# Kernel tuning notes

Measured on AMD Instinct MI355X. Metric: run time of the kernel, lower is better.

The kernel has to match this reference:

```python
import jax, jax.numpy as jnp
import numpy as np

HEAD, STACK = 8, 2
EPS = 1e-5


def _ln2d(x):
    # F.layer_norm(x, x.size()[1:]): normalize over (seq, feature) jointly, no affine
    m = jnp.mean(x, axis=(1, 2), keepdims=True)
    v = jnp.var(x, axis=(1, 2), keepdims=True)
    return (x - m) / jnp.sqrt(v + EPS)


def setup_inputs() -> dict:
    key = jax.random.key(0)
    ks = jax.random.split(key, 8)
    B, S, V, E, D, C = 64, 1024, 8000, 200, 200, 31
    g = lambda k, shape, sc: (jax.random.normal(k, shape, jnp.float32) * sc)
    return dict(
        x=jax.random.randint(ks[0], (B, S), 0, V),
        embed=g(ks[1], (V, E), 0.02),
        pos=g(ks[2], (S, E), 0.02),
        Wp=g(ks[3], (E, D), 0.05), bp=jnp.zeros((D,), jnp.float32),
        Wm=g(ks[4], (D * HEAD, D), 0.05), bm=jnp.zeros((D,), jnp.float32),
        W1=g(ks[5], (D, D), 0.05), b1=jnp.zeros((D,), jnp.float32),
        W2=g(ks[6], (D, D), 0.05), b2=jnp.zeros((D,), jnp.float32),
        Wd=g(ks[7], (D, C), 0.05), bd=jnp.zeros((C,), jnp.float32),
    )


def reference(x, embed, pos, Wp, bp, Wm, bm, W1, b1, W2, b2, Wd, bd):
    h = embed[x] + pos                       # [B,S,200]
    scale = jnp.sqrt(jnp.asarray(Wp.shape[1], jnp.float32))
    for _ in range(STACK):                   # weights shared across stacks (aliased in torch)
        r = h
        p = h @ Wp + bp                      # q = k = v (same aliased Linear in torch)
        a = jax.nn.softmax(jnp.einsum('bsd,btd->bst', p, p) / scale, axis=-1)
        c = jnp.einsum('bst,btd->bsd', a, p)  # [B,S,200]
        cat = jnp.tile(c, (1, 1, HEAD))       # all heads identical -> concat = tile
        h = _ln2d(cat @ Wm + bm + r)
        r = h
        ff = jax.nn.relu(h @ W1 + b1) @ W2 + b2
        h = _ln2d(ff + r)
    return h[:, -1, :] @ Wd + bd             # [B, class_num]; dropout = identity (eval)
```

## Files before the change

kernel.cpp:

```cpp
#include <hip/hip_runtime.h>
#include <cstddef>
#include <cstdint>
#include <cmath>

#define BDIM  64
#define SDIM  1024
#define DDIM  200
#define DPAD  224
#define PSTRIDE 232
#define CDIM  31
#define NSTACK 2
#define EPS   1e-5f
#define LN_N  204800.0f

typedef __attribute__((ext_vector_type(8))) short short8;
typedef __attribute__((ext_vector_type(4))) short short4_t;
typedef __attribute__((ext_vector_type(4))) float f32x4;

__device__ __forceinline__ short f2bf(float f) {
    union { float f; unsigned u; } v; v.f = f;
    unsigned r = v.u + 0x7FFFu + ((v.u >> 16) & 1u);
    return (short)(r >> 16);
}
__device__ __forceinline__ float bf2f(short s) {
    union { unsigned u; float f; } v; v.u = ((unsigned)(unsigned short)s) << 16;
    return v.f;
}
__device__ __forceinline__ unsigned cvtpk_bf16(float a, float b) {
    unsigned r;
    asm volatile("v_cvt_pk_bf16_f32 %0, %1, %2" : "=v"(r) : "v"(a), "v"(b));
    return r;
}
__device__ __forceinline__ void gload_lds16(const short* g, short* l) {
    __builtin_amdgcn_global_load_lds(
        (const __attribute__((address_space(1))) void*)g,
        (__attribute__((address_space(3))) void*)l, 16, 0, 0);
}

__global__ void prep_kernel(const float* __restrict__ Wp, const float* __restrict__ bp,
                            const float* __restrict__ Wm, const float* __restrict__ bm,
                            const float* __restrict__ W1, const float* __restrict__ b1,
                            const float* __restrict__ W2, const float* __restrict__ b2,
                            short* __restrict__ WtP, short* __restrict__ WtM,
                            short* __restrict__ Wt1, short* __restrict__ Wt2,
                            float* __restrict__ bpP, float* __restrict__ bmP,
                            float* __restrict__ b1P, float* __restrict__ b2P,
                            float* __restrict__ csP, float* __restrict__ cs1)
{
    int idx = blockIdx.x * 256 + threadIdx.x;
    if (idx >= DPAD * DPAD) return;
    int n = idx / DPAD, k = idx - n * DPAD;
    bool valid = (n < DDIM) && (k < DDIM);
    WtP[idx] = valid ? f2bf(Wp[(size_t)k * DDIM + n]) : 0;
    Wt1[idx] = valid ? f2bf(W1[(size_t)k * DDIM + n]) : 0;
    Wt2[idx] = valid ? f2bf(W2[(size_t)k * DDIM + n]) : 0;
    float s = 0.f;
    if (valid) {
        #pragma unroll
        for (int blk = 0; blk < 8; ++blk)
            s += Wm[(size_t)(blk * DDIM + k) * DDIM + n];
    }
    WtM[idx] = valid ? f2bf(s) : 0;
    if (idx < DPAD) {
        bpP[idx] = idx < DDIM ? bp[idx] : 0.f;
        bmP[idx] = idx < DDIM ? bm[idx] : 0.f;
        b1P[idx] = idx < DDIM ? b1[idx] : 0.f;
        b2P[idx] = idx < DDIM ? b2[idx] : 0.f;
        float sp = 0.f, s1 = 0.f;
        if (idx < DDIM) {
            for (int kk = 0; kk < DDIM; ++kk) {
                sp += bf2f(f2bf(Wp[(size_t)kk * DDIM + idx]));
                s1 += bf2f(f2bf(W1[(size_t)kk * DDIM + idx]));
            }
        }
        csP[idx] = sp;
        cs1[idx] = s1;
    }
}

__global__ void embed_kernel(const int* __restrict__ x, const float* __restrict__ embed,
                             const float* __restrict__ pos, short* __restrict__ h)
{
    const int total = BDIM * SDIM * (DPAD / 4);
    for (int i = blockIdx.x * 256 + threadIdx.x; i < total; i += gridDim.x * 256) {
        const int row = i / (DPAD / 4);
        const int n0  = (i - row * (DPAD / 4)) * 4;
        short4_t o;
        if (n0 >= DDIM) {
            o[0] = o[1] = o[2] = o[3] = 0;
        } else {
            const int s = row & (SDIM - 1);
            const int tok = x[row];
            const float4 e  = *(const float4*)(embed + (size_t)tok * DDIM + n0);
            const float4 p4 = *(const float4*)(pos + (size_t)s * DDIM + n0);
            o[0] = f2bf(e.x + p4.x); o[1] = f2bf(e.y + p4.y);
            o[2] = f2bf(e.z + p4.z); o[3] = f2bf(e.w + p4.w);
        }
        *(short4_t*)(h + (size_t)row * DPAD + n0) = o;
    }
}

#define WSLICE 7168
__global__ __launch_bounds__(256, 3)
void gemm_bf(const short* __restrict__ act, const float* __restrict__ actParts,
             const short* __restrict__ Wt, const float* __restrict__ bias,
             const float* __restrict__ csW,
             const short* __restrict__ res, const float* __restrict__ resParts,
             short* __restrict__ out, float* __restrict__ parts,
             int doRelu, int outStride)
{
    __shared__ short WB[2][WSLICE];

    const int tid  = threadIdx.x;
    const int wave = tid >> 6, lane = tid & 63;
    const int lo   = lane & 15, hi = lane >> 4;
    const int mblk = blockIdx.x * 128;
    const int m0   = mblk + wave * 32;

    auto stage = [&](int ks, int buf) {
        for (int c = wave; c < 14; c += 4) {
            int row = c * 16 + (lane >> 2);
            int kc  = (lane & 3) ^ ((row >> 1) & 3);
            gload_lds16(Wt + (size_t)row * DPAD + ks * 32 + kc * 8,
                        &WB[buf][c * 512 + lane * 8]);
        }
    };

    f32x4 acc[2][14];
    #pragma unroll
    for (int mt = 0; mt < 2; ++mt)
        #pragma unroll
        for (int nt = 0; nt < 14; ++nt) acc[mt][nt] = (f32x4){0.f, 0.f, 0.f, 0.f};

    short8 af[2], afn[2];
    #pragma unroll
    for (int mt = 0; mt < 2; ++mt)
        af[mt] = *(const short8*)(act + (size_t)(m0 + mt * 16 + lo) * DPAD + hi * 8);
    stage(0, 0);
    __syncthreads();

    #pragma unroll
    for (int ks = 0; ks < 7; ++ks) {
        const int cur = ks & 1;
        if (ks < 6) {
            #pragma unroll
            for (int mt = 0; mt < 2; ++mt)
                afn[mt] = *(const short8*)(act + (size_t)(m0 + mt * 16 + lo) * DPAD
                                           + (ks + 1) * 32 + hi * 8);
            stage(ks + 1, cur ^ 1);
        }
        #pragma unroll
        for (int nt = 0; nt < 14; ++nt) {
            int brow = nt * 16 + lo;
            short8 bf_ = *(const short8*)&WB[cur][brow * 32
                                                  + ((hi * 8) ^ (((brow >> 1) & 3) << 3))];
            acc[0][nt] = __builtin_amdgcn_mfma_f32_16x16x32_bf16(af[0], bf_, acc[0][nt], 0, 0, 0);
            acc[1][nt] = __builtin_amdgcn_mfma_f32_16x16x32_bf16(af[1], bf_, acc[1][nt], 0, 0, 0);
        }
        __syncthreads();
        if (ks < 6) { af[0] = afn[0]; af[1] = afn[1]; }
    }

    const int bb = mblk >> 10;
    float inv_a = 1.f, corr = 0.f;
    if (actParts) {
        float mean = actParts[bb * 2] / LN_N;
        inv_a = rsqrtf(actParts[bb * 2 + 1] / LN_N - mean * mean + EPS);
        corr = mean * inv_a;
    }
    float mean_r = 0.f, inv_r = 1.f;
    if (resParts) {
        mean_r = resParts[bb * 2] / LN_N;
        inv_r = rsqrtf(resParts[bb * 2 + 1] / LN_N - mean_r * mean_r + EPS);
    }

    float s = 0.f, s2 = 0.f;
    #pragma unroll
    for (int mt = 0; mt < 2; ++mt) {
        #pragma unroll
        for (int nt = 0; nt < 14; ++nt) {
            const int n = nt * 16 + lo;
            const float bn = bias[n];
            const float cw = actParts ? csW[n] : 0.f;
            float v[4];
            #pragma unroll
            for (int r = 0; r < 4; ++r)
                v[r] = acc[mt][nt][r] * inv_a + bn - corr * cw;
            if (res) {
                #pragma unroll
                for (int r = 0; r < 4; ++r) {
                    int m = m0 + mt * 16 + hi * 4 + r;
                    v[r] += (bf2f(res[(size_t)m * DPAD + n]) - mean_r) * inv_r;
                }
            }
            if (doRelu)
                #pragma unroll
                for (int r = 0; r < 4; ++r) v[r] = fmaxf(v[r], 0.f);
            if (n >= DDIM)
                #pragma unroll
                for (int r = 0; r < 4; ++r) v[r] = 0.f;
            if (parts)
                #pragma unroll
                for (int r = 0; r < 4; ++r) { s += v[r]; s2 = fmaf(v[r], v[r], s2); }
            #pragma unroll
            for (int r = 0; r < 4; ++r) {
                int m = m0 + mt * 16 + hi * 4 + r;
                out[(size_t)m * outStride + n] = f2bf(v[r]);
            }
        }
    }

    if (parts) {
        __shared__ float rs[4], rq[4];
        #pragma unroll
        for (int off = 32; off; off >>= 1) {
            s  += __shfl_down(s, off);
            s2 += __shfl_down(s2, off);
        }
        if (lane == 0) { rs[wave] = s; rq[wave] = s2; }
        __syncthreads();
        if (tid == 0) {
            atomicAdd(&parts[bb * 2],     rs[0] + rs[1] + rs[2] + rs[3]);
            atomicAdd(&parts[bb * 2 + 1], rq[0] + rq[1] + rq[2] + rq[3]);
        }
    }
}

#define Y1S 232
__global__ __launch_bounds__(256, 2)
void ffn_bf(const short* __restrict__ act, const float* __restrict__ actParts,
            const float* __restrict__ csW1,
            const short* __restrict__ Wt1, const float* __restrict__ b1,
            const short* __restrict__ Wt2, const float* __restrict__ b2,
            short* __restrict__ out, float* __restrict__ parts)
{
    __shared__ short WB[2][WSLICE];
    __shared__ short Y1[64 * Y1S];

    const int tid  = threadIdx.x;
    const int wave = tid >> 6, lane = tid & 63;
    const int lo   = lane & 15, hi = lane >> 4;
    const int mblk = blockIdx.x * 64;
    const int m0   = mblk + wave * 16;
    const int bb   = mblk >> 10;

    auto stageW = [&](const short* W, int ks, int buf) {
        for (int c = wave; c < 14; c += 4) {
            int row = c * 16 + (lane >> 2);
            int kc  = (lane & 3) ^ ((row >> 1) & 3);
            gload_lds16(W + (size_t)row * DPAD + ks * 32 + kc * 8,
                        &WB[buf][c * 512 + lane * 8]);
        }
    };

    const float mean_a = actParts[bb * 2] / LN_N;
    const float inv_a  = rsqrtf(actParts[bb * 2 + 1] / LN_N - mean_a * mean_a + EPS);
    const float corr   = mean_a * inv_a;

    f32x4 acc[14];
    #pragma unroll
    for (int nt = 0; nt < 14; ++nt) acc[nt] = (f32x4){0.f, 0.f, 0.f, 0.f};

    short8 af = *(const short8*)(act + (size_t)(m0 + lo) * DPAD + hi * 8);
    short8 afn;
    stageW(Wt1, 0, 0);
    __syncthreads();

    #pragma unroll
    for (int ks = 0; ks < 7; ++ks) {
        const int cur = ks & 1;
        if (ks < 6) {
            afn = *(const short8*)(act + (size_t)(m0 + lo) * DPAD + (ks + 1) * 32 + hi * 8);
            stageW(Wt1, ks + 1, cur ^ 1);
        } else {
            stageW(Wt2, 0, cur ^ 1);
        }
        #pragma unroll
        for (int nt = 0; nt < 14; ++nt) {
            int brow = nt * 16 + lo;
            short8 bf_ = *(const short8*)&WB[cur][brow * 32
                                                  + ((hi * 8) ^ (((brow >> 1) & 3) << 3))];
            acc[nt] = __builtin_amdgcn_mfma_f32_16x16x32_bf16(af, bf_, acc[nt], 0, 0, 0);
        }
        __syncthreads();
        if (ks < 6) af = afn;
    }

    #pragma unroll
    for (int nt = 0; nt < 14; ++nt) {
        const int n = nt * 16 + lo;
        const float bn = b1[n];
        const float cw = csW1[n];
        #pragma unroll
        for (int r = 0; r < 4; ++r) {
            float v = fmaxf(acc[nt][r] * inv_a + bn - corr * cw, 0.f);
            Y1[(wave * 16 + hi * 4 + r) * Y1S + n] = f2bf(v);
        }
    }
    __syncthreads();

    #pragma unroll
    for (int nt = 0; nt < 14; ++nt) acc[nt] = (f32x4){0.f, 0.f, 0.f, 0.f};

    #pragma unroll
    for (int ks = 0; ks < 7; ++ks) {
        const int cur = (ks + 1) & 1;
        if (ks < 6) stageW(Wt2, ks + 1, cur ^ 1);
        short8 a2 = *(const short8*)&Y1[(wave * 16 + lo) * Y1S + ks * 32 + hi * 8];
        #pragma unroll
        for (int nt = 0; nt < 14; ++nt) {
            int brow = nt * 16 + lo;
            short8 bf_ = *(const short8*)&WB[cur][brow * 32
                                                  + ((hi * 8) ^ (((brow >> 1) & 3) << 3))];
            acc[nt] = __builtin_amdgcn_mfma_f32_16x16x32_bf16(a2, bf_, acc[nt], 0, 0, 0);
        }
        __syncthreads();
    }

    float s = 0.f, s2 = 0.f;
    #pragma unroll
    for (int nt = 0; nt < 14; ++nt) {
        const int n = nt * 16 + lo;
        const float bn = b2[n];
        float v[4];
        #pragma unroll
        for (int r = 0; r < 4; ++r) {
            int m = m0 + hi * 4 + r;
            v[r] = acc[nt][r] + bn + (bf2f(act[(size_t)m * DPAD + n]) - mean_a) * inv_a;
        }
        if (n >= DDIM)
            #pragma unroll
            for (int r = 0; r < 4; ++r) v[r] = 0.f;
        #pragma unroll
        for (int r = 0; r < 4; ++r) { s += v[r]; s2 = fmaf(v[r], v[r], s2); }
        #pragma unroll
        for (int r = 0; r < 4; ++r) {
            int m = m0 + hi * 4 + r;
            out[(size_t)m * DPAD + n] = f2bf(v[r]);
        }
    }

    {
        __shared__ float rs[4], rq[4];
        #pragma unroll
        for (int off = 32; off; off >>= 1) {
            s  += __shfl_down(s, off);
            s2 += __shfl_down(s2, off);
        }
        if (lane == 0) { rs[wave] = s; rq[wave] = s2; }
        __syncthreads();
        if (tid == 0) {
            atomicAdd(&parts[bb * 2],     rs[0] + rs[1] + rs[2] + rs[3]);
            atomicAdd(&parts[bb * 2 + 1], rq[0] + rq[1] + rq[2] + rq[3]);
        }
    }
}

__global__ void vt_kernel(const short* __restrict__ p, short* __restrict__ pt)
{
    __shared__ short T[32][33];
    const int b  = blockIdx.z;
    const int s0 = blockIdx.x * 32;
    const int d0 = blockIdx.y * 32;
    const int t  = threadIdx.x;
    const int row = t >> 3, c4 = (t & 7) * 4;
    short4_t v = *(const short4_t*)(p + ((size_t)b * SDIM + s0 + row) * PSTRIDE + d0 + c4);
    #pragma unroll
    for (int j = 0; j < 4; ++j) T[row][c4 + j] = v[j];
    __syncthreads();
    short4_t o;
    #pragma unroll
    for (int j = 0; j < 4; ++j) o[j] = T[c4 + j][row];
    *(short4_t*)(pt + ((size_t)b * DPAD + d0 + row) * SDIM + s0 + c4) = o;
}

__global__ __launch_bounds__(256, 2)
void attn_kernel(const short* __restrict__ pbf, const short* __restrict__ pt,
                 short* __restrict__ c, float qscale)
{
    __shared__ short Kbuf[2][7680];
    __shared__ short Vbuf[2][6656];

    const int bid = blockIdx.x;
    const int wg  = (bid & 7) * 64 + (bid >> 3);
    const int b   = wg >> 3;
    const int q0  = (wg & 7) * 128;

    const int tid  = threadIdx.x;
    const int wave = tid >> 6;
    const int lane = tid & 63;
    const int lo   = lane & 15;
    const int hi   = lane >> 4;

    const short* pb  = pbf + (size_t)b * SDIM * PSTRIDE;
    const short* ptb = pt  + (size_t)b * DPAD * SDIM;

    auto stage = [&](int kt2, int bufIdx) {
        const short* ks = pb + (size_t)kt2 * 32 * PSTRIDE + lane * 8;
        #pragma unroll
        for (int i = 0; i < 15; ++i)
            gload_lds16(ks + i * 512, &Kbuf[bufIdx][i * 512]);
        #pragma unroll
        for (int i = 0; i < 13; ++i) {
            int e = i * 512 + lane * 8;
            int d = e >> 5;
            int cc = (e & 31) ^ (((d >> 1) & 3) << 3);
            gload_lds16(ptb + (size_t)d * SDIM + kt2 * 32 + cc, &Vbuf[bufIdx][i * 512]);
        }
    };

    short8 qf[2][7];
    #pragma unroll
    for (int qt = 0; qt < 2; ++qt)
        #pragma unroll
        for (int ks = 0; ks < 7; ++ks) {
            short8 q = *(const short8*)(pb + (size_t)(q0 + wave * 32 + qt * 16 + lo) * PSTRIDE
                                        + ks * 32 + hi * 8);
            short8 qs;
            #pragma unroll
            for (int j = 0; j < 8; ++j) qs[j] = f2bf(bf2f(q[j]) * qscale);
            qf[qt][ks] = qs;
        }

    f32x4 o[2][13];
    float m[2], ell[2];
    #pragma unroll
    for (int qt = 0; qt < 2; ++qt) {
        #pragma unroll
        for (int n = 0; n < 13; ++n) o[qt][n] = (f32x4){0.f, 0.f, 0.f, 0.f};
        m[qt] = -1e30f; ell[qt] = 0.f;
    }

    if (wave == 0) stage(0, 0);
    __syncthreads();

    for (int kt = 0; kt < 32; ++kt) {
        const int cur = kt & 1;
        if (kt < 31 && wave == ((kt + 1) & 3)) stage(kt + 1, cur ^ 1);

        f32x4 sacc[2][2];
        #pragma unroll
        for (int qt = 0; qt < 2; ++qt)
            #pragma unroll
            for (int t = 0; t < 2; ++t) sacc[qt][t] = (f32x4){0.f, 0.f, 0.f, 0.f};
        __builtin_amdgcn_s_setprio(1);
        #pragma unroll
        for (int t = 0; t < 2; ++t)
            #pragma unroll
            for (int ks = 0; ks < 7; ++ks) {
                short8 kf = *(const short8*)(&Kbuf[cur][(t * 16 + lo) * PSTRIDE + ks * 32 + hi * 8]);
                sacc[0][t] = __builtin_amdgcn_mfma_f32_16x16x32_bf16(kf, qf[0][ks], sacc[0][t], 0, 0, 0);
                sacc[1][t] = __builtin_amdgcn_mfma_f32_16x16x32_bf16(kf, qf[1][ks], sacc[1][t], 0, 0, 0);
            }
        __builtin_amdgcn_s_setprio(0);

        short8 pa[2];
        #pragma unroll
        for (int qt = 0; qt < 2; ++qt) {
            float mx = fmaxf(fmaxf(fmaxf(sacc[qt][0][0], sacc[qt][0][1]),
                                   fmaxf(sacc[qt][0][2], sacc[qt][0][3])),
                             fmaxf(fmaxf(sacc[qt][1][0], sacc[qt][1][1]),
                                   fmaxf(sacc[qt][1][2], sacc[qt][1][3])));
            mx = fmaxf(mx, __shfl_xor(mx, 16));
            mx = fmaxf(mx, __shfl_xor(mx, 32));
            if (__any(mx > m[qt] + 11.5f)) {
                float mn = fmaxf(m[qt], mx);
                float al = exp2f(m[qt] - mn);
                m[qt] = mn; ell[qt] *= al;
                float alr[4];
                #pragma unroll
                for (int r = 0; r < 4; ++r) alr[r] = __shfl(al, hi * 4 + r);
                #pragma unroll
                for (int n = 0; n < 13; ++n)
                    #pragma unroll
                    for (int r = 0; r < 4; ++r) o[qt][n][r] *= alr[r];
            }
            float p[2][4]; float rsum = 0.f;
            #pragma unroll
            for (int t = 0; t < 2; ++t)
                #pragma unroll
                for (int r = 0; r < 4; ++r) {
                    p[t][r] = exp2f(sacc[qt][t][r] - m[qt]);
                    rsum += p[t][r];
                }
            rsum += __shfl_xor(rsum, 16);
            rsum += __shfl_xor(rsum, 32);
            ell[qt] += rsum;
            unsigned pk01_0 = cvtpk_bf16(p[0][0], p[0][1]);
            unsigned pk23_0 = cvtpk_bf16(p[0][2], p[0][3]);
            unsigned pk01_1 = cvtpk_bf16(p[1][0], p[1][1]);
            unsigned pk23_1 = cvtpk_bf16(p[1][2], p[1][3]);
            const int srcA = lo + ((hi & 1) * 2) * 16;
            const int srcB = srcA + 16;
            int a0 = __shfl((int)pk01_0, srcA), a1 = __shfl((int)pk01_1, srcA);
            int b0 = __shfl((int)pk23_0, srcA), b1 = __shfl((int)pk23_1, srcA);
            int c0 = __shfl((int)pk01_0, srcB), c1 = __shfl((int)pk01_1, srcB);
            int d0 = __shfl((int)pk23_0, srcB), d1 = __shfl((int)pk23_1, srcB);
            const bool thi = (hi >> 1) != 0;
            union { short8 s; int u[4]; } pu;
            pu.u[0] = thi ? a1 : a0;
            pu.u[1] = thi ? b1 : b0;
            pu.u[2] = thi ? c1 : c0;
            pu.u[3] = thi ? d1 : d0;
            pa[qt] = pu.s;
        }

        __builtin_amdgcn_s_setprio(1);
        #pragma unroll
        for (int n = 0; n < 13; ++n) {
            int d = n * 16 + lo;
            int addr = d * 32 + ((hi * 8) ^ (((d >> 1) & 3) << 3));
            short8 vf = *(const short8*)(&Vbuf[cur][addr]);
            o[0][n] = __builtin_amdgcn_mfma_f32_16x16x32_bf16(pa[0], vf, o[0][n], 0, 0, 0);
            o[1][n] = __builtin_amdgcn_mfma_f32_16x16x32_bf16(pa[1], vf, o[1][n], 0, 0, 0);
        }
        __builtin_amdgcn_s_setprio(0);

        __syncthreads();
    }

    #pragma unroll
    for (int qt = 0; qt < 2; ++qt) {
        float inv_l = 1.f / ell[qt];
        float invr[4];
        #pragma unroll
        for (int r = 0; r < 4; ++r) invr[r] = __shfl(inv_l, hi * 4 + r);
        #pragma unroll
        for (int n = 0; n < 13; ++n) {
            int dcol = n * 16 + lo;
            #pragma unroll
            for (int r = 0; r < 4; ++r) {
                size_t row = (size_t)b * SDIM + q0 + wave * 32 + qt * 16 + hi * 4 + r;
                c[row * DPAD + dcol] = f2bf(o[qt][n][r] * invr[r]);
            }
        }
        #pragma unroll
        for (int r = 0; r < 4; ++r) {
            size_t row = (size_t)b * SDIM + q0 + wave * 32 + qt * 16 + hi * 4 + r;
            c[row * DPAD + 208 + lo] = 0;
        }
    }
}

__global__ void final_kernel(const short* __restrict__ y, const float* __restrict__ parts,
                             const float* __restrict__ Wd, const float* __restrict__ bd,
                             float* __restrict__ out)
{
    const int b = blockIdx.x;
    const float sum = parts[b * 2], sq = parts[b * 2 + 1];
    const float mean = sum / LN_N;
    const float inv  = rsqrtf(sq / LN_N - mean * mean + EPS);
    __shared__ float hrow[DDIM];
    const short* row = y + ((size_t)b * SDIM + SDIM - 1) * DPAD;
    for (int d = threadIdx.x; d < DDIM; d += blockDim.x)
        hrow[d] = (bf2f(row[d]) - mean) * inv;
    __syncthreads();
    if (threadIdx.x < CDIM) {
        float acc = bd[threadIdx.x];
        for (int d = 0; d < DDIM; ++d)
            acc = fmaf(hrow[d], Wd[(size_t)d * CDIM + threadIdx.x], acc);
        out[(size_t)b * CDIM + threadIdx.x] = acc;
    }
}

extern "C" void kernel_launch(void* const* d_in, const int* in_sizes, int n_in,
                              void* d_out, int out_size, void* d_ws, size_t ws_size,
                              hipStream_t stream)
{
    const int*   x     = (const int*)  d_in[0];
    const float* embed = (const float*)d_in[1];
    const float* pos   = (const float*)d_in[2];
    const float* Wp    = (const float*)d_in[3];
    const float* bp    = (const float*)d_in[4];
    const float* Wm    = (const float*)d_in[5];
    const float* bm    = (const float*)d_in[6];
    const float* W1    = (const float*)d_in[7];
    const float* b1    = (const float*)d_in[8];
    const float* W2    = (const float*)d_in[9];
    const float* b2    = (const float*)d_in[10];
    const float* Wd    = (const float*)d_in[11];
    const float* bd    = (const float*)d_in[12];
    float* out = (float*)d_out;

    const size_t HB = (size_t)BDIM * SDIM * DPAD;
    const size_t PB = (size_t)BDIM * SDIM * PSTRIDE;

    short* h_bf  = (short*)d_ws;
    short* p_bf  = h_bf  + HB;
    short* pt    = p_bf  + PB;
    short* cb_bf = pt    + HB;
    short* yA    = cb_bf + HB;
    short* yB    = yA    + HB;
    short* WtP   = yB + HB;
    short* WtM   = WtP + DPAD * DPAD;
    short* Wt1   = WtM + DPAD * DPAD;
    short* Wt2   = Wt1 + DPAD * DPAD;
    float* bpP   = (float*)(Wt2 + DPAD * DPAD);
    float* bmP   = bpP + DPAD;
    float* b1P   = bmP + DPAD;
    float* b2P   = b1P + DPAD;
    float* csP   = b2P + DPAD;
    float* cs1   = csP + DPAD;
    float* parts = cs1 + DPAD;
    const size_t need = (size_t)((char*)(parts + 4 * BDIM * 2) - (char*)d_ws);
    if (ws_size < need) return;

    float* pA1 = parts;
    float* pB1 = parts + BDIM * 2;
    float* pA2 = parts + 2 * BDIM * 2;
    float* pB2 = parts + 3 * BDIM * 2;

    prep_kernel<<<dim3((DPAD * DPAD + 255) / 256), dim3(256), 0, stream>>>(
        Wp, bp, Wm, bm, W1, b1, W2, b2, WtP, WtM, Wt1, Wt2, bpP, bmP, b1P, b2P, csP, cs1);
    embed_kernel<<<dim3(2048), dim3(256), 0, stream>>>(x, embed, pos, h_bf);
    hipMemsetAsync(parts, 0, 4 * BDIM * 2 * sizeof(float), stream);

    const float qscale = 1.44269504f / sqrtf((float)DDIM);
    const dim3 tgrid(SDIM / 32, DPAD / 32, BDIM);

    gemm_bf<<<dim3(512), dim3(256), 0, stream>>>(h_bf, nullptr, WtP, bpP, nullptr,
                                                 nullptr, nullptr, p_bf, nullptr, 0, PSTRIDE);
    vt_kernel<<<tgrid, dim3(256), 0, stream>>>(p_bf, pt);
    attn_kernel<<<dim3(512), dim3(256), 0, stream>>>(p_bf, pt, cb_bf, qscale);
    gemm_bf<<<dim3(512), dim3(256), 0, stream>>>(cb_bf, nullptr, WtM, bmP, nullptr,
                                                 h_bf, nullptr, yA, pA1, 0, DPAD);
    ffn_bf<<<dim3(1024), dim3(256), 0, stream>>>(yA, pA1, cs1, Wt1, b1P, Wt2, b2P, yB, pB1);
    gemm_bf<<<dim3(512), dim3(256), 0, stream>>>(yB, pB1, WtP, bpP, csP,
                                                 nullptr, nullptr, p_bf, nullptr, 0, PSTRIDE);
    vt_kernel<<<tgrid, dim3(256), 0, stream>>>(p_bf, pt);
    attn_kernel<<<dim3(512), dim3(256), 0, stream>>>(p_bf, pt, cb_bf, qscale);
    gemm_bf<<<dim3(512), dim3(256), 0, stream>>>(cb_bf, nullptr, WtM, bmP, nullptr,
                                                 yB, pB1, h_bf, pA2, 0, DPAD);
    ffn_bf<<<dim3(1024), dim3(256), 0, stream>>>(h_bf, pA2, cs1, Wt1, b1P, Wt2, b2P, yA, pB2);
    final_kernel<<<dim3(BDIM), dim3(64), 0, stream>>>(yA, pB2, Wd, bd, out);
}
```

Before: 398.0 us.

## Fuse transpose into projection GEMM epilogue and merge prep, embed, memset launches

The projection GEMM now also writes the transposed P layout directly from its epilogue as short4 column stores, which removes the separate vt_kernel transpose pass and its extra read of P. The weight prep, embedding gather and the partial-sum memset are folded into one launch through block-index dispatch, cutting two launches. The transposed stores are strided (one short4 per 2 KB row), so write efficiency may be poor. The guard nt < 13 may leave the padded columns 208-223 of pt unwritten.

```diff
diff --git a/kernel.cpp b/kernel.cpp
--- a/kernel.cpp
+++ b/kernel.cpp
@@ -12,6 +12,7 @@
 #define NSTACK 2
 #define EPS   1e-5f
 #define LN_N  204800.0f
+#define PREP_BLOCKS 196
 
 typedef __attribute__((ext_vector_type(8))) short short8;
 typedef __attribute__((ext_vector_type(4))) short short4_t;
@@ -37,52 +38,58 @@
         (__attribute__((address_space(3))) void*)l, 16, 0, 0);
 }
 
-__global__ void prep_kernel(const float* __restrict__ Wp, const float* __restrict__ bp,
-                            const float* __restrict__ Wm, const float* __restrict__ bm,
-                            const float* __restrict__ W1, const float* __restrict__ b1,
-                            const float* __restrict__ W2, const float* __restrict__ b2,
-                            short* __restrict__ WtP, short* __restrict__ WtM,
-                            short* __restrict__ Wt1, short* __restrict__ Wt2,
-                            float* __restrict__ bpP, float* __restrict__ bmP,
-                            float* __restrict__ b1P, float* __restrict__ b2P,
-                            float* __restrict__ csP, float* __restrict__ cs1)
+__global__ void prep_embed_kernel(const int* __restrict__ x, const float* __restrict__ embed,
+                                  const float* __restrict__ pos,
+                                  const float* __restrict__ Wp, const float* __restrict__ bp,
+                                  const float* __restrict__ Wm, const float* __restrict__ bm,
+                                  const float* __restrict__ W1, const float* __restrict__ b1,
+                                  const float* __restrict__ W2, const float* __restrict__ b2,
+                                  short* __restrict__ WtP, short* __restrict__ WtM,
+                                  short* __restrict__ Wt1, short* __restrict__ Wt2,
+                                  float* __restrict__ bpP, float* __restrict__ bmP,
+                                  float* __restrict__ b1P, float* __restrict__ b2P,
+                                  float* __restrict__ csP, float* __restrict__ cs1,
+                                  short* __restrict__ h, float* __restrict__ parts)
 {
-    int idx = blockIdx.x * 256 + threadIdx.x;
-    if (idx >= DPAD * DPAD) return;
-    int n = idx / DPAD, k = idx - n * DPAD;
-    bool valid = (n < DDIM) && (k < DDIM);
-    WtP[idx] = valid ? f2bf(Wp[(size_t)k * DDIM + n]) : 0;
-    Wt1[idx] = valid ? f2bf(W1[(size_t)k * DDIM + n]) : 0;
-    Wt2[idx] = valid ? f2bf(W2[(size_t)k * DDIM + n]) : 0;
-    float s = 0.f;
-    if (valid) {
-        #pragma unroll
-        for (int blk = 0; blk < 8; ++blk)
-            s += Wm[(size_t)(blk * DDIM + k) * DDIM + n];
-    }
-    WtM[idx] = valid ? f2bf(s) : 0;
-    if (idx < DPAD) {
-        bpP[idx] = idx < DDIM ? bp[idx] : 0.f;
-        bmP[idx] = idx < DDIM ? bm[idx] : 0.f;
-        b1P[idx] = idx < DDIM ? b1[idx] : 0.f;
-        b2P[idx] = idx < DDIM ? b2[idx] : 0.f;
-        float sp = 0.f, s1 = 0.f;
-        if (idx < DDIM) {
-            for (int kk = 0; kk < DDIM; ++kk) {
-                sp += bf2f(f2bf(Wp[(size_t)kk * DDIM + idx]));
-                s1 += bf2f(f2bf(W1[(size_t)kk * DDIM + idx]));
+    if (blockIdx.x < PREP_BLOCKS) {
+        int idx = blockIdx.x * 256 + threadIdx.x;
+        if (idx >= DPAD * DPAD) return;
+        int n = idx / DPAD, k = idx - n * DPAD;
+        bool valid = (n < DDIM) && (k < DDIM);
+        WtP[idx] = valid ? f2bf(Wp[(size_t)k * DDIM + n]) : 0;
+        Wt1[idx] = valid ? f2bf(W1[(size_t)k * DDIM + n]) : 0;
+        Wt2[idx] = valid ? f2bf(W2[(size_t)k * DDIM + n]) : 0;
+        float s = 0.f;
+        if (valid) {
+            #pragma unroll
+            for (int blk = 0; blk < 8; ++blk)
+                s += Wm[(size_t)(blk * DDIM + k) * DDIM + n];
+        }
+        WtM[idx] = valid ? f2bf(s) : 0;
+        if (idx < DPAD) {
+            bpP[idx] = idx < DDIM ? bp[idx] : 0.f;
+            bmP[idx] = idx < DDIM ? bm[idx] : 0.f;
+            b1P[idx] = idx < DDIM ? b1[idx] : 0.f;
+            b2P[idx] = idx < DDIM ? b2[idx] : 0.f;
+            float sp = 0.f, s1 = 0.f;
+            if (idx < DDIM) {
+                for (int kk = 0; kk < DDIM; ++kk) {
+                    sp += bf2f(f2bf(Wp[(size_t)kk * DDIM + idx]));
+                    s1 += bf2f(f2bf(W1[(size_t)kk * DDIM + idx]));
+                }
             }
-        }
-        csP[idx] = sp;
-        cs1[idx] = s1;
-    }
-}
-
-__global__ void embed_kernel(const int* __restrict__ x, const float* __restrict__ embed,
-                             const float* __restrict__ pos, short* __restrict__ h)
-{
+            csP[idx] = sp;
+            cs1[idx] = s1;
+        }
+        return;
+    }
+
+    const int eb = blockIdx.x - PREP_BLOCKS;
+    if (eb == 0) {
+        for (int i = threadIdx.x; i < 4 * BDIM * 2; i += 256) parts[i] = 0.f;
+    }
     const int total = BDIM * SDIM * (DPAD / 4);
-    for (int i = blockIdx.x * 256 + threadIdx.x; i < total; i += gridDim.x * 256) {
+    for (int i = eb * 256 + threadIdx.x; i < total; i += 2048 * 256) {
         const int row = i / (DPAD / 4);
         const int n0  = (i - row * (DPAD / 4)) * 4;
         short4_t o;
@@ -106,8 +113,8 @@
              const short* __restrict__ Wt, const float* __restrict__ bias,
              const float* __restrict__ csW,
              const short* __restrict__ res, const float* __restrict__ resParts,
-             short* __restrict__ out, float* __restrict__ parts,
-             int doRelu, int outStride)
+             short* __restrict__ out, short* __restrict__ pt,
+             float* __restrict__ parts, int doRelu, int outStride)
 {
     __shared__ short WB[2][WSLICE];
 
@@ -202,10 +209,17 @@
             if (parts)
                 #pragma unroll
                 for (int r = 0; r < 4; ++r) { s += v[r]; s2 = fmaf(v[r], v[r], s2); }
+            short4_t o4;
+            #pragma unroll
+            for (int r = 0; r < 4; ++r) o4[r] = f2bf(v[r]);
             #pragma unroll
             for (int r = 0; r < 4; ++r) {
                 int m = m0 + mt * 16 + hi * 4 + r;
-                out[(size_t)m * outStride + n] = f2bf(v[r]);
+                out[(size_t)m * outStride + n] = o4[r];
+            }
+            if (pt && nt < 13) {
+                const int sloc = (m0 + mt * 16 + hi * 4) & (SDIM - 1);
+                *(short4_t*)(pt + ((size_t)bb * DPAD + n) * SDIM + sloc) = o4;
             }
         }
     }
@@ -354,24 +368,6 @@
             atomicAdd(&parts[bb * 2 + 1], rq[0] + rq[1] + rq[2] + rq[3]);
         }
     }
-}
-
-__global__ void vt_kernel(const short* __restrict__ p, short* __restrict__ pt)
-{
-    __shared__ short T[32][33];
-    const int b  = blockIdx.z;
-    const int s0 = blockIdx.x * 32;
-    const int d0 = blockIdx.y * 32;
-    const int t  = threadIdx.x;
-    const int row = t >> 3, c4 = (t & 7) * 4;
-    short4_t v = *(const short4_t*)(p + ((size_t)b * SDIM + s0 + row) * PSTRIDE + d0 + c4);
-    #pragma unroll
-    for (int j = 0; j < 4; ++j) T[row][c4 + j] = v[j];
-    __syncthreads();
-    short4_t o;
-    #pragma unroll
-    for (int j = 0; j < 4; ++j) o[j] = T[c4 + j][row];
-    *(short4_t*)(pt + ((size_t)b * DPAD + d0 + row) * SDIM + s0 + c4) = o;
 }
 
 __global__ __launch_bounds__(256, 2)
@@ -610,27 +606,23 @@
     float* pA2 = parts + 2 * BDIM * 2;
     float* pB2 = parts + 3 * BDIM * 2;
 
-    prep_kernel<<<dim3((DPAD * DPAD + 255) / 256), dim3(256), 0, stream>>>(
-        Wp, bp, Wm, bm, W1, b1, W2, b2, WtP, WtM, Wt1, Wt2, bpP, bmP, b1P, b2P, csP, cs1);
-    embed_kernel<<<dim3(2048), dim3(256), 0, stream>>>(x, embed, pos, h_bf);
-    hipMemsetAsync(parts, 0, 4 * BDIM * 2 * sizeof(float), stream);
+    prep_embed_kernel<<<dim3(PREP_BLOCKS + 2048), dim3(256), 0, stream>>>(
+        x, embed, pos, Wp, bp, Wm, bm, W1, b1, W2, b2,
+        WtP, WtM, Wt1, Wt2, bpP, bmP, b1P, b2P, csP, cs1, h_bf, parts);
 
     const float qscale = 1.44269504f / sqrtf((float)DDIM);
-    const dim3 tgrid(SDIM / 32, DPAD / 32, BDIM);
 
     gemm_bf<<<dim3(512), dim3(256), 0, stream>>>(h_bf, nullptr, WtP, bpP, nullptr,
-                                                 nullptr, nullptr, p_bf, nullptr, 0, PSTRIDE);
-    vt_kernel<<<tgrid, dim3(256), 0, stream>>>(p_bf, pt);
+                                                 nullptr, nullptr, p_bf, pt, nullptr, 0, PSTRIDE);
     attn_kernel<<<dim3(512), dim3(256), 0, stream>>>(p_bf, pt, cb_bf, qscale);
     gemm_bf<<<dim3(512), dim3(256), 0, stream>>>(cb_bf, nullptr, WtM, bmP, nullptr,
-                                                 h_bf, nullptr, yA, pA1, 0, DPAD);
+                                                 h_bf, nullptr, yA, nullptr, pA1, 0, DPAD);
     ffn_bf<<<dim3(1024), dim3(256), 0, stream>>>(yA, pA1, cs1, Wt1, b1P, Wt2, b2P, yB, pB1);
     gemm_bf<<<dim3(512), dim3(256), 0, stream>>>(yB, pB1, WtP, bpP, csP,
-                                                 nullptr, nullptr, p_bf, nullptr, 0, PSTRIDE);
-    vt_kernel<<<tgrid, dim3(256), 0, stream>>>(p_bf, pt);
+                                                 nullptr, nullptr, p_bf, pt, nullptr, 0, PSTRIDE);
     attn_kernel<<<dim3(512), dim3(256), 0, stream>>>(p_bf, pt, cb_bf, qscale);
     gemm_bf<<<dim3(512), dim3(256), 0, stream>>>(cb_bf, nullptr, WtM, bmP, nullptr,
-                                                 yB, pB1, h_bf, pA2, 0, DPAD);
+                                                 yB, pB1, h_bf, nullptr, pA2, 0, DPAD);
     ffn_bf<<<dim3(1024), dim3(256), 0, stream>>>(h_bf, pA2, cs1, Wt1, b1P, Wt2, b2P, yA, pB2);
     final_kernel<<<dim3(BDIM), dim3(64), 0, stream>>>(yA, pB2, Wd, bd, out);
 }
```

After: 382.0 us. -4.0%, faster.
